# Performance work log

Measured on AMD Instinct MI355X. Metric: run time of the kernel, lower is better.

The kernel has to match this reference:

```python
import jax, jax.numpy as jnp
import numpy as np

DIM = 256
HEADS = 8
HEAD_DIM = DIM // HEADS
B = 8
HH, WW = 32, 32
N = HH * WW
TABLE = (2 * HH - 1) * (2 * WW - 1)  # 3969
CPB_HID = 512


def _l2norm(t, eps=1e-12):
    # matches torch F.normalize(dim=-1): x / max(||x||, eps)
    n = jnp.sqrt(jnp.sum(t * t, axis=-1, keepdims=True))
    return t / jnp.maximum(n, eps)


def setup_inputs() -> dict:
    key = jax.random.key(0)
    ks = jax.random.split(key, 12)
    x = jax.random.normal(ks[0], (B, N, DIM), dtype=jnp.float32)
    relative_pos_index = jax.random.randint(ks[1], (N, N), 0, TABLE)
    relative_coords_table = jax.random.normal(ks[2], (TABLE, 2), dtype=jnp.float32)
    s = 0.02
    qkv_w = jax.random.normal(ks[3], (3 * DIM, DIM), dtype=jnp.float32) * s
    qkv_b = jnp.zeros((3 * DIM,), dtype=jnp.float32)
    query_embedding = jax.random.normal(ks[4], (HEADS, 1, HEAD_DIM), dtype=jnp.float32) * s
    # temperature init: log(exp(1/0.24) - 1) so softplus(temperature) = 1/0.24
    temperature = jnp.full((HEADS, 1, 1), float(np.log(np.expm1(1.0 / 0.24))), dtype=jnp.float32)
    proj_w = jax.random.normal(ks[5], (DIM, DIM), dtype=jnp.float32) * s
    proj_b = jnp.zeros((DIM,), dtype=jnp.float32)
    cpb_fc1_w = jax.random.normal(ks[6], (CPB_HID, 2), dtype=jnp.float32) * s
    cpb_fc1_b = jnp.zeros((CPB_HID,), dtype=jnp.float32)
    cpb_fc2_w = jax.random.normal(ks[7], (HEADS, CPB_HID), dtype=jnp.float32) * s
    cpb_fc2_b = jnp.zeros((HEADS,), dtype=jnp.float32)
    return dict(x=x, H=HH, W=WW, relative_pos_index=relative_pos_index,
                relative_coords_table=relative_coords_table,
                qkv_w=qkv_w, qkv_b=qkv_b, query_embedding=query_embedding,
                temperature=temperature, proj_w=proj_w, proj_b=proj_b,
                cpb_fc1_w=cpb_fc1_w, cpb_fc1_b=cpb_fc1_b,
                cpb_fc2_w=cpb_fc2_w, cpb_fc2_b=cpb_fc2_b)


def reference(x, H, W, relative_pos_index, relative_coords_table,
              qkv_w, qkv_b, query_embedding, temperature,
              proj_w, proj_b, cpb_fc1_w, cpb_fc1_b, cpb_fc2_w, cpb_fc2_b):
    Bc, Nc, C = x.shape
    seq_length_scale = jnp.asarray(np.log(HH * WW), dtype=x.dtype)  # from init input_resolution
    # qkv projection -> [B, heads, N, head_dim] each
    qkv = (x @ qkv_w.T + qkv_b).reshape(Bc, Nc, 3 * HEADS, HEAD_DIM).transpose(0, 2, 1, 3)
    q, k, v = qkv[:, :HEADS], qkv[:, HEADS:2 * HEADS], qkv[:, 2 * HEADS:]
    # CPB relative position bias: small MLP over coord table, then NxN gather
    h = jax.nn.relu(relative_coords_table @ cpb_fc1_w.T + cpb_fc1_b)  # [T, 512]
    table = (h @ cpb_fc2_w.T + cpb_fc2_b).T                           # [heads, T]
    rel_bias = table[:, relative_pos_index.reshape(-1)].reshape(HEADS, Nc, Nc)
    # cosine attention with learned temperature
    qn = _l2norm(q) + query_embedding[None]                           # [B, heads, N, hd]
    scale = jax.nn.softplus(temperature) * seq_length_scale           # [heads, 1, 1]
    attn = jnp.einsum('bhnd,bhmd->bhnm', qn * scale[None], _l2norm(k)) + rel_bias[None]
    attn = jax.nn.softmax(attn, axis=-1)
    out = jnp.einsum('bhnm,bhmd->bhnd', attn, v).transpose(0, 2, 1, 3).reshape(Bc, Nc, C)
    return out @ proj_w.T + proj_b
```

## Files before the change

### kernel.cpp

```cpp
#include <hip/hip_runtime.h>
#include <hip/hip_bf16.h>
#include <cstddef>
#include <cstdint>

typedef float v4f __attribute__((ext_vector_type(4)));
typedef short v8s __attribute__((ext_vector_type(8)));
typedef _Float16 v8h __attribute__((ext_vector_type(8)));

__device__ __forceinline__ uint32_t fbits(float x){ uint32_t u; __builtin_memcpy(&u,&x,4); return u; }
__device__ __forceinline__ float ffrom(uint32_t u){ float f; __builtin_memcpy(&f,&u,4); return f; }
__device__ __forceinline__ short bf_rh(float x){ return (short)((fbits(x)+0x8000u)>>16); }
__device__ __forceinline__ uint32_t pack_bf_rh(float a, float b){
    uint32_t ua = fbits(a)+0x8000u, ub = fbits(b)+0x8000u;
#if __has_builtin(__builtin_amdgcn_perm)
    return __builtin_amdgcn_perm(ub, ua, 0x07060302u);
#else
    return (ua>>16) | (ub & 0xFFFF0000u);
#endif
}
__device__ __forceinline__ short f2h(float x){ _Float16 h = (_Float16)x; short s; __builtin_memcpy(&s,&h,2); return s; }
#if __has_builtin(__builtin_amdgcn_exp2f)
#define EXP2(x) __builtin_amdgcn_exp2f(x)
#else
#define EXP2(x) exp2f(x)
#endif

__device__ __forceinline__ void gld16(const void* g, void* l) {
    __builtin_amdgcn_global_load_lds(
        (const __attribute__((address_space(1))) unsigned int*)g,
        (__attribute__((address_space(3))) unsigned int*)l, 16, 0, 0);
}
#define MFMA(a,b,c)  __builtin_amdgcn_mfma_f32_16x16x32_bf16((a),(b),(c),0,0,0)
#define MFMAH(a,b,c) __builtin_amdgcn_mfma_f32_16x16x32_f16((a),(b),(c),0,0,0)

#define LOG2E 1.4426950408889634f

__global__ __launch_bounds__(256)
void cpb_kernel(const float* __restrict__ rct,
                const float* __restrict__ fc1w, const float* __restrict__ fc1b,
                const float* __restrict__ fc2w, const float* __restrict__ fc2b,
                float* __restrict__ table)
{
    __shared__ float s1[1024];
    __shared__ float sb[512];
    __shared__ float s2[4096];
    int tid = threadIdx.x;
    for (int i = tid; i < 1024; i += 256) s1[i] = fc1w[i];
    for (int i = tid; i < 512;  i += 256) sb[i] = fc1b[i];
    for (int i = tid; i < 4096; i += 256) s2[i] = fc2w[i];
    __syncthreads();
    int rl = tid >> 2, jp = tid & 3;
    bool ok = rl < 63;
    int r = blockIdx.x * 63 + rl;
    float c0 = ok ? rct[2*r]   : 0.f;
    float c1 = ok ? rct[2*r+1] : 0.f;
    float a[8] = {0,0,0,0,0,0,0,0};
    int j0 = jp * 128;
    #pragma unroll 4
    for (int j = j0; j < j0 + 128; ++j) {
        float hv = fmaxf(c0*s1[2*j] + c1*s1[2*j+1] + sb[j], 0.0f);
        #pragma unroll
        for (int hh = 0; hh < 8; ++hh) a[hh] += hv * s2[hh*512 + j];
    }
    #pragma unroll
    for (int hh = 0; hh < 8; ++hh) {
        a[hh] += __shfl_xor(a[hh], 1);
        a[hh] += __shfl_xor(a[hh], 2);
    }
    if (ok && jp == 0) {
        #pragma unroll
        for (int hh = 0; hh < 8; ++hh) table[hh*3969 + r] = a[hh] + fc2b[hh];
    }
}

__global__ __launch_bounds__(256)
void bias_mat(const float* __restrict__ tblf, const int* __restrict__ rpi,
              short* __restrict__ biasM)
{
    __shared__ float tb[3969];
    int h   = blockIdx.x >> 6;
    int q16 = blockIdx.x & 63;
    int tid = threadIdx.x;
    int w = tid >> 6, lane = tid & 63, t = lane & 15, quad = lane >> 4;
    for (int i = tid; i < 3969; i += 256) tb[i] = tblf[h*3969 + i] * LOG2E;
    __syncthreads();
    int row0 = q16*16 + quad*4;
    #pragma unroll 1
    for (int kk = 0; kk < 4; ++kk) {
        int kt = w*4 + kk;
        #pragma unroll
        for (int g = 0; g < 4; ++g) {
            float o[4];
            #pragma unroll
            for (int r = 0; r < 4; ++r)
                o[r] = tb[rpi[(size_t)(row0 + r)*1024 + kt*64 + 4*t + g]];
            uint2 pk;
            pk.x = pack_bf_rh(o[0], o[1]);
            pk.y = pack_bf_rh(o[2], o[3]);
            size_t base = ((((size_t)(h*64 + q16)*16 + kt)*4 + g)*64 + lane)*4;
            *(uint2*)(biasM + base) = pk;
        }
    }
}

__global__ __launch_bounds__(256)
void split_kernel(const float* __restrict__ x,  short* __restrict__ xh,
                  const float* __restrict__ wq, short* __restrict__ wqh,
                  const float* __restrict__ wp, short* __restrict__ wph)
{
    int bid = blockIdx.x;
    const float* src; short* dh; int base8;
    if (bid < 1024)      { src = x;  dh = xh;  base8 = bid * 256; }
    else if (bid < 1120) { src = wq; dh = wqh; base8 = (bid-1024) * 256; }
    else                 { src = wp; dh = wph; base8 = (bid-1120) * 256; }
    int e0 = (base8 + (int)threadIdx.x) * 8;
    int m  = e0 >> 8;
    int k  = e0 & 255;
    int kt = k >> 6, c = (k >> 3) & 7;
    float4 f0 = *(const float4*)(src + e0);
    float4 f1 = *(const float4*)(src + e0 + 4);
    float v[8] = {f0.x,f0.y,f0.z,f0.w,f1.x,f1.y,f1.z,f1.w};
    v8s hi;
    #pragma unroll
    for (int j = 0; j < 8; ++j) hi[j] = f2h(v[j]);
    int dst = m*256 + kt*64 + ((c ^ (m & 7)) << 3);
    *(v8s*)&dh[dst] = hi;
}

template<int MODE>
__global__ __launch_bounds__(256)
void gemm_mfma(const short* __restrict__ Ah_g, const short* __restrict__ Wh_g,
               const float* __restrict__ bias, float* __restrict__ C,
               short* __restrict__ qh, short* __restrict__ kh,
               short* __restrict__ vt,
               const float* __restrict__ qe, const float* __restrict__ temp,
               int N)
{
    __shared__ __align__(16) char smem[49152];
    short* A0 = (short*)smem;
    short* A1 = A0 + 128*64;
    short* W0 = A1 + 128*64;
    short* W1 = W0 + 64*64;

    int tid  = threadIdx.x;
    int w    = tid >> 6;
    int lane = tid & 63;
    int t    = lane & 15;
    int quad = lane >> 4;
    int m0 = blockIdx.y * 128, n0 = blockIdx.x * 64;
    int Mw = (w >> 1) * 64, Nw = (w & 1) * 32;

    v4f acc[4][2];
    #pragma unroll
    for (int mt = 0; mt < 4; ++mt)
        #pragma unroll
        for (int nt = 0; nt < 2; ++nt) acc[mt][nt] = (v4f){0,0,0,0};

    int lr8 = lane >> 3, lc8 = lane & 7;
    #pragma unroll 1
    for (int kt2 = 0; kt2 < 2; ++kt2) {
        __syncthreads();
        #pragma unroll
        for (int half = 0; half < 2; ++half) {
            int kt = kt2*2 + half;
            short* Ad = half ? A1 : A0;
            short* Wd = half ? W1 : W0;
            #pragma unroll
            for (int i = 0; i < 4; ++i) {
                size_t grow = (size_t)(m0 + w*32 + i*8 + lr8) * 256 + kt*64 + lc8*8;
                gld16(Ah_g + grow, Ad + (w*32 + i*8) * 64);
            }
            #pragma unroll
            for (int i = 0; i < 2; ++i) {
                size_t grow = (size_t)(n0 + w*16 + i*8 + lr8) * 256 + kt*64 + lc8*8;
                gld16(Wh_g + grow, Wd + (w*16 + i*8) * 64);
            }
        }
        __syncthreads();
        #pragma unroll
        for (int half = 0; half < 2; ++half) {
            const short* As = half ? A1 : A0;
            const short* Ws = half ? W1 : W0;
            #pragma unroll
            for (int kk = 0; kk < 2; ++kk) {
                int cp = ((kk*4 + quad) ^ (t & 7)) << 3;
                v8h bh8[2];
                #pragma unroll
                for (int nt = 0; nt < 2; ++nt)
                    bh8[nt] = *(const v8h*)&Ws[(Nw + nt*16 + t)*64 + cp];
                #pragma unroll
                for (int mt = 0; mt < 4; ++mt) {
                    v8h ah = *(const v8h*)&As[(Mw + mt*16 + t)*64 + cp];
                    #pragma unroll
                    for (int nt = 0; nt < 2; ++nt)
                        acc[mt][nt] = MFMAH(ah, bh8[nt], acc[mt][nt]);
                }
            }
        }
    }

    #pragma unroll
    for (int nt = 0; nt < 2; ++nt) {
        float bv = bias[n0 + Nw + nt*16 + t];
        #pragma unroll
        for (int mt = 0; mt < 4; ++mt)
            #pragma unroll
            for (int r = 0; r < 4; ++r) acc[mt][nt][r] += bv;
    }

    if (MODE == 0) {
        #pragma unroll
        for (int mt = 0; mt < 4; ++mt)
            #pragma unroll
            for (int r = 0; r < 4; ++r) {
                int m = m0 + Mw + mt*16 + quad*4 + r;
                #pragma unroll
                for (int nt = 0; nt < 2; ++nt)
                    C[(size_t)m * N + n0 + Nw + nt*16 + t] = acc[mt][nt][r];
            }
    } else {
        int which = n0 >> 8;
        if (which < 2) {
            int head = ((n0 + Nw) >> 5) & 7;
            float scale = 0.f;
            if (which == 0)
                scale = log1pf(__expf(temp[head])) * 10.0f;
            #pragma unroll
            for (int mt = 0; mt < 4; ++mt)
                #pragma unroll
                for (int r = 0; r < 4; ++r) {
                    float a0 = acc[mt][0][r], a1 = acc[mt][1][r];
                    float s = a0*a0 + a1*a1;
                    s += __shfl_xor(s, 1); s += __shfl_xor(s, 2);
                    s += __shfl_xor(s, 4); s += __shfl_xor(s, 8);
                    float inv = 1.0f / fmaxf(sqrtf(s), 1e-12f);
                    int m = m0 + Mw + mt*16 + quad*4 + r;
                    int b = m >> 10, nrow = m & 1023;
                    if (which == 0) {
                        size_t rowoff = (((size_t)b*8 + head)*1024 + nrow) * 32;
                        #pragma unroll
                        for (int nt = 0; nt < 2; ++nt) {
                            int d = nt*16 + t;
                            float val = (acc[mt][nt][r] * inv + qe[head*32 + d]) * scale;
                            qh[rowoff + d] = f2h(val);
                        }
                    } else {
                        int kk = nrow & 63;
                        int p  = (kk & 3)*16 + (kk >> 2);
                        int prow = (nrow & ~63) | p;
                        int swk = (kk >> 3) & 3;
                        size_t rowoff = (((size_t)b*8 + head)*1024 + prow) * 32;
                        #pragma unroll
                        for (int nt = 0; nt < 2; ++nt) {
                            int d = nt*16 + t;
                            int dpos = (((d >> 3) ^ swk) << 3) | (d & 7);
                            kh[rowoff + dpos] = f2h(acc[mt][nt][r] * inv);
                        }
                    }
                }
        } else {
            __syncthreads();
            short* VT = (short*)smem;
            #pragma unroll
            for (int mt = 0; mt < 4; ++mt)
                #pragma unroll
                for (int nt = 0; nt < 2; ++nt) {
                    int cl = Nw + nt*16 + t;
                    #pragma unroll
                    for (int r = 0; r < 4; ++r) {
                        int rl = Mw + mt*16 + quad*4 + r;
                        VT[cl*136 + rl] = bf_rh(acc[mt][nt][r]);
                    }
                }
            __syncthreads();
            int b = m0 >> 10;
            int keybase = m0 & 1023;
            int headbase = ((n0 - 512) >> 5) & 7;
            int cl = tid >> 2;
            int dim = cl & 31;
            int hd  = headbase + (cl >> 5);
            size_t obase = (((size_t)b*8 + hd)*32 + dim) * 1024 + keybase;
            #pragma unroll
            for (int p = 0; p < 4; ++p) {
                int ci  = (tid & 3) * 4 + p;
                int ktl = ci >> 3, c = ci & 7;
                v8s val = *(const v8s*)&VT[cl*136 + ktl*64 + c*8];
                *(v8s*)&vt[obase + ktl*64 + ((c ^ (dim & 7)) << 3)] = val;
            }
        }
    }
}

__global__ __launch_bounds__(256)
void attn_mfma(const short* __restrict__ qh, const short* __restrict__ kh,
               const short* __restrict__ vt,  const short* __restrict__ biasM,
               short* __restrict__ yh)
{
    __shared__ __align__(16) short Kh_s[2][2048];
    __shared__ __align__(16) short Vt_s[2][2048];
    __shared__ __align__(16) short Ps[4][16][68];

    int bh  = blockIdx.x >> 4;
    int qt  = blockIdx.x & 15;
    int h   = bh & 7;
    int b   = bh >> 3;
    int tid = threadIdx.x;
    int w    = tid >> 6;
    int lane = tid & 63;
    int t    = lane & 15;
    int quad = lane >> 4;

    size_t qoff = ((size_t)bh*1024 + qt*64 + w*16 + t) * 32 + quad*8;
    v8h qf = *(const v8h*)(qh + qoff);

    v4f Oacc[2] = {{0,0,0,0},{0,0,0,0}};
    float lsum[4] = {0,0,0,0};

    size_t kgbase = (size_t)bh * 32768;
    const short* bmb = biasM + ((size_t)(h*64 + qt*4 + w) * 16) * 1024 + lane*4;
    int qrow0 = qt*64 + w*16 + quad*4;
    int swzS = (quad ^ ((t >> 1) & 3)) << 3;
    int lr8 = lane >> 3, lc8 = lane & 7;

    gld16(kh + kgbase + w*512 + lane*8, &Kh_s[0][w*512]);
    gld16(vt + kgbase + (size_t)(w*8 + lr8)*1024 + lc8*8, &Vt_s[0][w*512]);
    uint2 curb[4];
    #pragma unroll
    for (int g = 0; g < 4; ++g) curb[g] = *(const uint2*)(bmb + g*256);

    #pragma unroll 1
    for (int kt = 0; kt < 16; ++kt) {
        int cur = kt & 1;
        __syncthreads();
        uint2 nxtb[4];
        if (kt < 15) {
            int nkt = kt + 1, nb = cur ^ 1;
            gld16(kh + kgbase + (size_t)nkt*2048 + w*512 + lane*8, &Kh_s[nb][w*512]);
            gld16(vt + kgbase + (size_t)(w*8 + lr8)*1024 + nkt*64 + lc8*8, &Vt_s[nb][w*512]);
            const short* bp = bmb + (size_t)nkt*1024;
            #pragma unroll
            for (int g = 0; g < 4; ++g) nxtb[g] = *(const uint2*)(bp + g*256);
        }

        v4f S[4];
        #pragma unroll
        for (int g = 0; g < 4; ++g) {
            v8h kb = *(const v8h*)&Kh_s[cur][(g*16 + t)*32 + swzS];
            v4f c;
            c[0] = ffrom(curb[g].x << 16);
            c[1] = ffrom(curb[g].x & 0xFFFF0000u);
            c[2] = ffrom(curb[g].y << 16);
            c[3] = ffrom(curb[g].y & 0xFFFF0000u);
            S[g] = MFMAH(qf, kb, c);
        }

        #pragma unroll
        for (int r = 0; r < 4; ++r) {
            float p0 = EXP2(S[0][r]);
            float p1 = EXP2(S[1][r]);
            float p2 = EXP2(S[2][r]);
            float p3 = EXP2(S[3][r]);
            lsum[r] += (p0 + p1) + (p2 + p3);
            uint2 pk;
            pk.x = pack_bf_rh(p0, p1);
            pk.y = pack_bf_rh(p2, p3);
            *(uint2*)&Ps[w][quad*4 + r][t*4] = pk;
        }

        #pragma unroll
        for (int ks = 0; ks < 2; ++ks) {
            v8s pf = *(const v8s*)&Ps[w][t][ks*32 + quad*8];
            int vsw = ((ks*4 + quad) ^ (t & 7)) << 3;
            #pragma unroll
            for (int g = 0; g < 2; ++g) {
                v8s vf = *(const v8s*)&Vt_s[cur][(g*16 + t)*64 + vsw];
                Oacc[g] = MFMA(pf, vf, Oacc[g]);
            }
        }
        #pragma unroll
        for (int g = 0; g < 4; ++g) curb[g] = nxtb[g];
    }

    #pragma unroll
    for (int r = 0; r < 4; ++r) {
        float l = lsum[r];
        l += __shfl_xor(l, 1); l += __shfl_xor(l, 2);
        l += __shfl_xor(l, 4); l += __shfl_xor(l, 8);
        float inv = 1.0f / l;
        int qrow = qrow0 + r;
        int m = b*1024 + qrow;
        size_t mbase = (size_t)m * 256;
        int mk = m & 7;
        #pragma unroll
        for (int g = 0; g < 2; ++g) {
            float o = Oacc[g][r] * inv;
            int c = h*4 + g*2 + (t >> 3);
            int chp = ((c ^ mk) << 3) | (t & 7);
            yh[mbase + chp] = f2h(o);
        }
    }
}

extern "C" void kernel_launch(void* const* d_in, const int* in_sizes, int n_in,
                              void* d_out, int out_size, void* d_ws, size_t ws_size,
                              hipStream_t stream)
{
    const float* x     = (const float*)d_in[0];
    const int*   rpi   = (const int*)d_in[3];
    const float* rct   = (const float*)d_in[4];
    const float* qkvw  = (const float*)d_in[5];
    const float* qkvb  = (const float*)d_in[6];
    const float* qe    = (const float*)d_in[7];
    const float* temp  = (const float*)d_in[8];
    const float* projw = (const float*)d_in[9];
    const float* projb = (const float*)d_in[10];
    const float* fc1w  = (const float*)d_in[11];
    const float* fc1b  = (const float*)d_in[12];
    const float* fc2w  = (const float*)d_in[13];
    const float* fc2b  = (const float*)d_in[14];

    char* p = (char*)d_ws;
    float* tblf  = (float*)p;  p += 131072;
    short* xh    = (short*)p;  p += 4194304;
    short* wqh   = (short*)p;  p += 393216;
    short* wph   = (short*)p;  p += 131072;
    short* qh    = (short*)p;  p += 4194304;
    short* kh    = (short*)p;  p += 4194304;
    short* vt    = (short*)p;  p += 4194304;
    short* biasM = (short*)p;  p += 16777216;
    float* out   = (float*)d_out;

    cpb_kernel<<<63, 256, 0, stream>>>(rct, fc1w, fc1b, fc2w, fc2b, tblf);

    bias_mat<<<512, 256, 0, stream>>>(tblf, rpi, biasM);

    split_kernel<<<1152, 256, 0, stream>>>(x, xh, qkvw, wqh, projw, wph);

    dim3 g1(768/64, 8192/128);
    gemm_mfma<1><<<g1, 256, 0, stream>>>(xh, wqh, qkvb, nullptr,
                                         qh, kh, vt, qe, temp, 768);

    attn_mfma<<<1024, 256, 0, stream>>>(qh, kh, vt, biasM, xh);

    dim3 g2(256/64, 8192/128);
    gemm_mfma<0><<<g2, 256, 0, stream>>>(xh, wph, projb, out,
                                         nullptr, nullptr, nullptr,
                                         nullptr, nullptr, 256);
}
```

Measured before the change: 161.2 us.

## Merge prep kernels into fewer launches and shrink proj GEMM tiles

Merges the CPB MLP into the fp16 conversion kernel, and the bias-matrix gather into the QKV GEMM kernel, as extra blocks of one launch each. This cuts six launches to four and lets independent work share the GPU. The output projection gets its own kernel with 64x64 tiles, which doubles the block count so more CUs are busy. The cost is larger combined kernels whose shared-memory and register use follows the heavier branch, which may lower occupancy for the lighter blocks.

```diff
diff --git a/kernel.cpp b/kernel.cpp
--- a/kernel.cpp
+++ b/kernel.cpp
@@ -36,189 +36,150 @@
 #define LOG2E 1.4426950408889634f
 
 __global__ __launch_bounds__(256)
-void cpb_kernel(const float* __restrict__ rct,
-                const float* __restrict__ fc1w, const float* __restrict__ fc1b,
-                const float* __restrict__ fc2w, const float* __restrict__ fc2b,
-                float* __restrict__ table)
+void prep_kernel(const float* __restrict__ x,  short* __restrict__ xh,
+                 const float* __restrict__ wq, short* __restrict__ wqh,
+                 const float* __restrict__ wp, short* __restrict__ wph,
+                 const float* __restrict__ rct,
+                 const float* __restrict__ fc1w, const float* __restrict__ fc1b,
+                 const float* __restrict__ fc2w, const float* __restrict__ fc2b,
+                 float* __restrict__ table)
 {
     __shared__ float s1[1024];
     __shared__ float sb[512];
     __shared__ float s2[4096];
+    int bid = blockIdx.x;
     int tid = threadIdx.x;
-    for (int i = tid; i < 1024; i += 256) s1[i] = fc1w[i];
-    for (int i = tid; i < 512;  i += 256) sb[i] = fc1b[i];
-    for (int i = tid; i < 4096; i += 256) s2[i] = fc2w[i];
-    __syncthreads();
-    int rl = tid >> 2, jp = tid & 3;
-    bool ok = rl < 63;
-    int r = blockIdx.x * 63 + rl;
-    float c0 = ok ? rct[2*r]   : 0.f;
-    float c1 = ok ? rct[2*r+1] : 0.f;
-    float a[8] = {0,0,0,0,0,0,0,0};
-    int j0 = jp * 128;
-    #pragma unroll 4
-    for (int j = j0; j < j0 + 128; ++j) {
-        float hv = fmaxf(c0*s1[2*j] + c1*s1[2*j+1] + sb[j], 0.0f);
-        #pragma unroll
-        for (int hh = 0; hh < 8; ++hh) a[hh] += hv * s2[hh*512 + j];
+    if (bid < 1152) {
+        const float* src; short* dh; int base8;
+        if (bid < 1024)      { src = x;  dh = xh;  base8 = bid * 256; }
+        else if (bid < 1120) { src = wq; dh = wqh; base8 = (bid-1024) * 256; }
+        else                 { src = wp; dh = wph; base8 = (bid-1120) * 256; }
+        int e0 = (base8 + tid) * 8;
+        int m  = e0 >> 8;
+        int k  = e0 & 255;
+        int kt = k >> 6, c = (k >> 3) & 7;
+        float4 f0 = *(const float4*)(src + e0);
+        float4 f1 = *(const float4*)(src + e0 + 4);
+        float v[8] = {f0.x,f0.y,f0.z,f0.w,f1.x,f1.y,f1.z,f1.w};
+        v8s hi;
+        #pragma unroll
+        for (int j = 0; j < 8; ++j) hi[j] = f2h(v[j]);
+        int dst = m*256 + kt*64 + ((c ^ (m & 7)) << 3);
+        *(v8s*)&dh[dst] = hi;
+    } else {
+        int cbid = bid - 1152;
+        for (int i = tid; i < 1024; i += 256) s1[i] = fc1w[i];
+        for (int i = tid; i < 512;  i += 256) sb[i] = fc1b[i];
+        for (int i = tid; i < 4096; i += 256) s2[i] = fc2w[i];
+        __syncthreads();
+        int rl = tid >> 2, jp = tid & 3;
+        bool ok = rl < 63;
+        int r = cbid * 63 + rl;
+        float c0 = ok ? rct[2*r]   : 0.f;
+        float c1 = ok ? rct[2*r+1] : 0.f;
+        float a[8] = {0,0,0,0,0,0,0,0};
+        int j0 = jp * 128;
+        #pragma unroll 4
+        for (int j = j0; j < j0 + 128; ++j) {
+            float hv = fmaxf(c0*s1[2*j] + c1*s1[2*j+1] + sb[j], 0.0f);
+            #pragma unroll
+            for (int hh = 0; hh < 8; ++hh) a[hh] += hv * s2[hh*512 + j];
+        }
+        #pragma unroll
+        for (int hh = 0; hh < 8; ++hh) {
+            a[hh] += __shfl_xor(a[hh], 1);
+            a[hh] += __shfl_xor(a[hh], 2);
+        }
+        if (ok && jp == 0) {
+            #pragma unroll
+            for (int hh = 0; hh < 8; ++hh) table[hh*3969 + r] = a[hh] + fc2b[hh];
+        }
     }
-    #pragma unroll
-    for (int hh = 0; hh < 8; ++hh) {
-        a[hh] += __shfl_xor(a[hh], 1);
-        a[hh] += __shfl_xor(a[hh], 2);
-    }
-    if (ok && jp == 0) {
-        #pragma unroll
-        for (int hh = 0; hh < 8; ++hh) table[hh*3969 + r] = a[hh] + fc2b[hh];
-    }
 }
 
 __global__ __launch_bounds__(256)
-void bias_mat(const float* __restrict__ tblf, const int* __restrict__ rpi,
-              short* __restrict__ biasM)
-{
-    __shared__ float tb[3969];
-    int h   = blockIdx.x >> 6;
-    int q16 = blockIdx.x & 63;
-    int tid = threadIdx.x;
-    int w = tid >> 6, lane = tid & 63, t = lane & 15, quad = lane >> 4;
-    for (int i = tid; i < 3969; i += 256) tb[i] = tblf[h*3969 + i] * LOG2E;
-    __syncthreads();
-    int row0 = q16*16 + quad*4;
-    #pragma unroll 1
-    for (int kk = 0; kk < 4; ++kk) {
-        int kt = w*4 + kk;
-        #pragma unroll
-        for (int g = 0; g < 4; ++g) {
-            float o[4];
-            #pragma unroll
-            for (int r = 0; r < 4; ++r)
-                o[r] = tb[rpi[(size_t)(row0 + r)*1024 + kt*64 + 4*t + g]];
-            uint2 pk;
-            pk.x = pack_bf_rh(o[0], o[1]);
-            pk.y = pack_bf_rh(o[2], o[3]);
-            size_t base = ((((size_t)(h*64 + q16)*16 + kt)*4 + g)*64 + lane)*4;
-            *(uint2*)(biasM + base) = pk;
-        }
-    }
-}
-
-__global__ __launch_bounds__(256)
-void split_kernel(const float* __restrict__ x,  short* __restrict__ xh,
-                  const float* __restrict__ wq, short* __restrict__ wqh,
-                  const float* __restrict__ wp, short* __restrict__ wph)
-{
-    int bid = blockIdx.x;
-    const float* src; short* dh; int base8;
-    if (bid < 1024)      { src = x;  dh = xh;  base8 = bid * 256; }
-    else if (bid < 1120) { src = wq; dh = wqh; base8 = (bid-1024) * 256; }
-    else                 { src = wp; dh = wph; base8 = (bid-1120) * 256; }
-    int e0 = (base8 + (int)threadIdx.x) * 8;
-    int m  = e0 >> 8;
-    int k  = e0 & 255;
-    int kt = k >> 6, c = (k >> 3) & 7;
-    float4 f0 = *(const float4*)(src + e0);
-    float4 f1 = *(const float4*)(src + e0 + 4);
-    float v[8] = {f0.x,f0.y,f0.z,f0.w,f1.x,f1.y,f1.z,f1.w};
-    v8s hi;
-    #pragma unroll
-    for (int j = 0; j < 8; ++j) hi[j] = f2h(v[j]);
-    int dst = m*256 + kt*64 + ((c ^ (m & 7)) << 3);
-    *(v8s*)&dh[dst] = hi;
-}
-
-template<int MODE>
-__global__ __launch_bounds__(256)
-void gemm_mfma(const short* __restrict__ Ah_g, const short* __restrict__ Wh_g,
-               const float* __restrict__ bias, float* __restrict__ C,
-               short* __restrict__ qh, short* __restrict__ kh,
-               short* __restrict__ vt,
-               const float* __restrict__ qe, const float* __restrict__ temp,
-               int N)
+void qkv_bias_kernel(const short* __restrict__ xh, const short* __restrict__ wqh,
+                     const float* __restrict__ qkvb,
+                     short* __restrict__ qh, short* __restrict__ kh,
+                     short* __restrict__ vt,
+                     const float* __restrict__ qe, const float* __restrict__ temp,
+                     const float* __restrict__ tblf, const int* __restrict__ rpi,
+                     short* __restrict__ biasM)
 {
     __shared__ __align__(16) char smem[49152];
-    short* A0 = (short*)smem;
-    short* A1 = A0 + 128*64;
-    short* W0 = A1 + 128*64;
-    short* W1 = W0 + 64*64;
-
+    int bid  = blockIdx.x;
     int tid  = threadIdx.x;
     int w    = tid >> 6;
     int lane = tid & 63;
     int t    = lane & 15;
     int quad = lane >> 4;
-    int m0 = blockIdx.y * 128, n0 = blockIdx.x * 64;
-    int Mw = (w >> 1) * 64, Nw = (w & 1) * 32;
-
-    v4f acc[4][2];
-    #pragma unroll
-    for (int mt = 0; mt < 4; ++mt)
-        #pragma unroll
-        for (int nt = 0; nt < 2; ++nt) acc[mt][nt] = (v4f){0,0,0,0};
-
-    int lr8 = lane >> 3, lc8 = lane & 7;
-    #pragma unroll 1
-    for (int kt2 = 0; kt2 < 2; ++kt2) {
-        __syncthreads();
-        #pragma unroll
-        for (int half = 0; half < 2; ++half) {
-            int kt = kt2*2 + half;
-            short* Ad = half ? A1 : A0;
-            short* Wd = half ? W1 : W0;
-            #pragma unroll
-            for (int i = 0; i < 4; ++i) {
-                size_t grow = (size_t)(m0 + w*32 + i*8 + lr8) * 256 + kt*64 + lc8*8;
-                gld16(Ah_g + grow, Ad + (w*32 + i*8) * 64);
-            }
-            #pragma unroll
-            for (int i = 0; i < 2; ++i) {
-                size_t grow = (size_t)(n0 + w*16 + i*8 + lr8) * 256 + kt*64 + lc8*8;
-                gld16(Wh_g + grow, Wd + (w*16 + i*8) * 64);
-            }
-        }
-        __syncthreads();
-        #pragma unroll
-        for (int half = 0; half < 2; ++half) {
-            const short* As = half ? A1 : A0;
-            const short* Ws = half ? W1 : W0;
-            #pragma unroll
-            for (int kk = 0; kk < 2; ++kk) {
-                int cp = ((kk*4 + quad) ^ (t & 7)) << 3;
-                v8h bh8[2];
-                #pragma unroll
-                for (int nt = 0; nt < 2; ++nt)
-                    bh8[nt] = *(const v8h*)&Ws[(Nw + nt*16 + t)*64 + cp];
-                #pragma unroll
-                for (int mt = 0; mt < 4; ++mt) {
-                    v8h ah = *(const v8h*)&As[(Mw + mt*16 + t)*64 + cp];
+
+    if (bid < 768) {
+        short* A0 = (short*)smem;
+        short* A1 = A0 + 128*64;
+        short* W0 = A1 + 128*64;
+        short* W1 = W0 + 64*64;
+        int n0 = (bid % 12) * 64, m0 = (bid / 12) * 128;
+        int Mw = (w >> 1) * 64, Nw = (w & 1) * 32;
+
+        v4f acc[4][2];
+        #pragma unroll
+        for (int mt = 0; mt < 4; ++mt)
+            #pragma unroll
+            for (int nt = 0; nt < 2; ++nt) acc[mt][nt] = (v4f){0,0,0,0};
+
+        int lr8 = lane >> 3, lc8 = lane & 7;
+        #pragma unroll 1
+        for (int kt2 = 0; kt2 < 2; ++kt2) {
+            __syncthreads();
+            #pragma unroll
+            for (int half = 0; half < 2; ++half) {
+                int kt = kt2*2 + half;
+                short* Ad = half ? A1 : A0;
+                short* Wd = half ? W1 : W0;
+                #pragma unroll
+                for (int i = 0; i < 4; ++i) {
+                    size_t grow = (size_t)(m0 + w*32 + i*8 + lr8) * 256 + kt*64 + lc8*8;
+                    gld16(xh + grow, Ad + (w*32 + i*8) * 64);
+                }
+                #pragma unroll
+                for (int i = 0; i < 2; ++i) {
+                    size_t grow = (size_t)(n0 + w*16 + i*8 + lr8) * 256 + kt*64 + lc8*8;
+                    gld16(wqh + grow, Wd + (w*16 + i*8) * 64);
+                }
+            }
+            __syncthreads();
+            #pragma unroll
+            for (int half = 0; half < 2; ++half) {
+                const short* As = half ? A1 : A0;
+                const short* Ws = half ? W1 : W0;
+                #pragma unroll
+                for (int kk = 0; kk < 2; ++kk) {
+                    int cp = ((kk*4 + quad) ^ (t & 7)) << 3;
+                    v8h bh8[2];
                     #pragma unroll
                     for (int nt = 0; nt < 2; ++nt)
-                        acc[mt][nt] = MFMAH(ah, bh8[nt], acc[mt][nt]);
+                        bh8[nt] = *(const v8h*)&Ws[(Nw + nt*16 + t)*64 + cp];
+                    #pragma unroll
+                    for (int mt = 0; mt < 4; ++mt) {
+                        v8h ah = *(const v8h*)&As[(Mw + mt*16 + t)*64 + cp];
+                        #pragma unroll
+                        for (int nt = 0; nt < 2; ++nt)
+                            acc[mt][nt] = MFMAH(ah, bh8[nt], acc[mt][nt]);
+                    }
                 }
             }
         }
-    }
-
-    #pragma unroll
-    for (int nt = 0; nt < 2; ++nt) {
-        float bv = bias[n0 + Nw + nt*16 + t];
-        #pragma unroll
-        for (int mt = 0; mt < 4; ++mt)
-            #pragma unroll
-            for (int r = 0; r < 4; ++r) acc[mt][nt][r] += bv;
-    }
-
-    if (MODE == 0) {
-        #pragma unroll
-        for (int mt = 0; mt < 4; ++mt)
-            #pragma unroll
-            for (int r = 0; r < 4; ++r) {
-                int m = m0 + Mw + mt*16 + quad*4 + r;
-                #pragma unroll
-                for (int nt = 0; nt < 2; ++nt)
-                    C[(size_t)m * N + n0 + Nw + nt*16 + t] = acc[mt][nt][r];
-            }
-    } else {
+
+        #pragma unroll
+        for (int nt = 0; nt < 2; ++nt) {
+            float bv = qkvb[n0 + Nw + nt*16 + t];
+            #pragma unroll
+            for (int mt = 0; mt < 4; ++mt)
+                #pragma unroll
+                for (int r = 0; r < 4; ++r) acc[mt][nt][r] += bv;
+        }
+
         int which = n0 >> 8;
         if (which < 2) {
             int head = ((n0 + Nw) >> 5) & 7;
@@ -288,6 +249,30 @@
                 *(v8s*)&vt[obase + ktl*64 + ((c ^ (dim & 7)) << 3)] = val;
             }
         }
+    } else {
+        float* tb = (float*)smem;
+        int b2  = bid - 768;
+        int h   = b2 >> 6;
+        int q16 = b2 & 63;
+        for (int i = tid; i < 3969; i += 256) tb[i] = tblf[h*3969 + i] * LOG2E;
+        __syncthreads();
+        int row0 = q16*16 + quad*4;
+        #pragma unroll 1
+        for (int kk = 0; kk < 4; ++kk) {
+            int kt = w*4 + kk;
+            #pragma unroll
+            for (int g = 0; g < 4; ++g) {
+                float o[4];
+                #pragma unroll
+                for (int r = 0; r < 4; ++r)
+                    o[r] = tb[rpi[(size_t)(row0 + r)*1024 + kt*64 + 4*t + g]];
+                uint2 pk;
+                pk.x = pack_bf_rh(o[0], o[1]);
+                pk.y = pack_bf_rh(o[2], o[3]);
+                size_t base = ((((size_t)(h*64 + q16)*16 + kt)*4 + g)*64 + lane)*4;
+                *(uint2*)(biasM + base) = pk;
+            }
+        }
     }
 }
 
@@ -399,6 +384,85 @@
             yh[mbase + chp] = f2h(o);
         }
     }
+}
+
+__global__ __launch_bounds__(256)
+void gemm_proj(const short* __restrict__ Ah_g, const short* __restrict__ Wh_g,
+               const float* __restrict__ bias, float* __restrict__ C, int N)
+{
+    __shared__ __align__(16) short As[2][4096];
+    __shared__ __align__(16) short Ws[2][4096];
+
+    int tid  = threadIdx.x;
+    int w    = tid >> 6;
+    int lane = tid & 63;
+    int t    = lane & 15;
+    int quad = lane >> 4;
+    int m0 = blockIdx.y * 64, n0 = blockIdx.x * 64;
+    int Mw = (w >> 1) * 32, Nw = (w & 1) * 32;
+
+    v4f acc[2][2];
+    #pragma unroll
+    for (int mt = 0; mt < 2; ++mt)
+        #pragma unroll
+        for (int nt = 0; nt < 2; ++nt) acc[mt][nt] = (v4f){0,0,0,0};
+
+    int lr8 = lane >> 3, lc8 = lane & 7;
+    #pragma unroll 1
+    for (int kt2 = 0; kt2 < 2; ++kt2) {
+        __syncthreads();
+        #pragma unroll
+        for (int half = 0; half < 2; ++half) {
+            int kt = kt2*2 + half;
+            #pragma unroll
+            for (int i = 0; i < 2; ++i) {
+                size_t grow = (size_t)(m0 + w*16 + i*8 + lr8) * 256 + kt*64 + lc8*8;
+                gld16(Ah_g + grow, &As[half][(w*16 + i*8) * 64]);
+            }
+            #pragma unroll
+            for (int i = 0; i < 2; ++i) {
+                size_t grow = (size_t)(n0 + w*16 + i*8 + lr8) * 256 + kt*64 + lc8*8;
+                gld16(Wh_g + grow, &Ws[half][(w*16 + i*8) * 64]);
+            }
+        }
+        __syncthreads();
+        #pragma unroll
+        for (int half = 0; half < 2; ++half) {
+            #pragma unroll
+            for (int kk = 0; kk < 2; ++kk) {
+                int cp = ((kk*4 + quad) ^ (t & 7)) << 3;
+                v8h bh8[2];
+                #pragma unroll
+                for (int nt = 0; nt < 2; ++nt)
+                    bh8[nt] = *(const v8h*)&Ws[half][(Nw + nt*16 + t)*64 + cp];
+                #pragma unroll
+                for (int mt = 0; mt < 2; ++mt) {
+                    v8h ah = *(const v8h*)&As[half][(Mw + mt*16 + t)*64 + cp];
+                    #pragma unroll
+                    for (int nt = 0; nt < 2; ++nt)
+                        acc[mt][nt] = MFMAH(ah, bh8[nt], acc[mt][nt]);
+                }
+            }
+        }
+    }
+
+    #pragma unroll
+    for (int nt = 0; nt < 2; ++nt) {
+        float bv = bias[n0 + Nw + nt*16 + t];
+        #pragma unroll
+        for (int mt = 0; mt < 2; ++mt)
+            #pragma unroll
+            for (int r = 0; r < 4; ++r) acc[mt][nt][r] += bv;
+    }
+    #pragma unroll
+    for (int mt = 0; mt < 2; ++mt)
+        #pragma unroll
+        for (int r = 0; r < 4; ++r) {
+            int m = m0 + Mw + mt*16 + quad*4 + r;
+            #pragma unroll
+            for (int nt = 0; nt < 2; ++nt)
+                C[(size_t)m * N + n0 + Nw + nt*16 + t] = acc[mt][nt][r];
+        }
 }
 
 extern "C" void kernel_launch(void* const* d_in, const int* in_sizes, int n_in,
@@ -430,20 +494,14 @@
     short* biasM = (short*)p;  p += 16777216;
     float* out   = (float*)d_out;
 
-    cpb_kernel<<<63, 256, 0, stream>>>(rct, fc1w, fc1b, fc2w, fc2b, tblf);
-
-    bias_mat<<<512, 256, 0, stream>>>(tblf, rpi, biasM);
-
-    split_kernel<<<1152, 256, 0, stream>>>(x, xh, qkvw, wqh, projw, wph);
-
-    dim3 g1(768/64, 8192/128);
-    gemm_mfma<1><<<g1, 256, 0, stream>>>(xh, wqh, qkvb, nullptr,
-                                         qh, kh, vt, qe, temp, 768);
+    prep_kernel<<<1215, 256, 0, stream>>>(x, xh, qkvw, wqh, projw, wph,
+                                          rct, fc1w, fc1b, fc2w, fc2b, tblf);
+
+    qkv_bias_kernel<<<1280, 256, 0, stream>>>(xh, wqh, qkvb, qh, kh, vt,
+                                              qe, temp, tblf, rpi, biasM);
 
     attn_mfma<<<1024, 256, 0, stream>>>(qh, kh, vt, biasM, xh);
 
-    dim3 g2(256/64, 8192/128);
-    gemm_mfma<0><<<g2, 256, 0, stream>>>(xh, wph, projb, out,
-                                         nullptr, nullptr, nullptr,
-                                         nullptr, nullptr, 256);
-}
+    dim3 g2(256/64, 8192/64);
+    gemm_proj<<<g2, 256, 0, stream>>>(xh, wph, projb, out, 256);
+}
```

After: 152.2 us. 1.06x faster.
